# Kernel optimization log

Measured on AMD Instinct MI355X. Metric: run time of the kernel, lower is better.

The kernel has to match this reference:

```python
import jax, jax.numpy as jnp
import numpy as np

B, S, D, H = 4, 2048, 1024, 16
DH = D // H  # 64
R = 12       # random-projection rank forced by U's view()
EPS = 1e-6


def setup_inputs() -> dict:
    key = jax.random.key(0)
    ks = jax.random.split(key, 8)
    sc = 1.0 / np.sqrt(D)
    return {
        "Q": jax.random.normal(ks[0], (B, S, D), jnp.float32),
        "K": jax.random.normal(ks[1], (B, S, D), jnp.float32),
        "V": jax.random.normal(ks[2], (B, S, D), jnp.float32),
        "U": jax.random.normal(ks[3], (B, H, R, DH), jnp.float32),
        "W_Q": jax.random.normal(ks[4], (D, D), jnp.float32) * sc,
        "W_K": jax.random.normal(ks[5], (D, D), jnp.float32) * sc,
        "W_V": jax.random.normal(ks[6], (D, D), jnp.float32) * sc,
        "W_lin": jax.random.normal(ks[7], (D, D), jnp.float32) * sc,
        "b_lin": jnp.zeros((D,), jnp.float32),
        "gamma": jnp.ones((D,), jnp.float32),
        "beta": jnp.zeros((D,), jnp.float32),
    }


def reference(Q, K, V, U, W_Q, W_K, W_V, W_lin, b_lin, gamma, beta):
    b, s, d_model = Q.shape

    def proj(X, W):  # nn.Linear (no bias): X @ W^T, split heads -> [B,H,S,dh]
        return (X @ W.T).reshape(b, s, H, DH).transpose(0, 2, 1, 3)

    q = proj(Q, W_Q)
    k = proj(K, W_K)
    v = proj(V, W_V)

    # scores = (q @ U^T)^T @ k : random projection onto R=12 dims
    s1 = jnp.einsum('bhsd,bhrd->bhsr', q, U)          # [B,H,S,R]
    s2 = jnp.einsum('bhsr,bhsd->bhrd', s1, k)         # [B,H,R,dh]
    attn = jax.nn.softmax(s2, axis=-1)                # softmax over dh
    ctx = jnp.einsum('bhrd,bhsd->bhrs', attn, v)      # [B,H,R,S]
    # transpose(1,2) -> [B,R,H,S], flatten to [B, R*H*S/D, D]
    ctx = ctx.transpose(0, 2, 1, 3).reshape(b, -1, d_model)

    out = ctx @ W_lin.T + b_lin                       # final linear
    # dropout is identity in eval mode; then LayerNorm(eps=1e-6)
    mu = jnp.mean(out, axis=-1, keepdims=True)
    var = jnp.var(out, axis=-1, keepdims=True)
    return (out - mu) * jax.lax.rsqrt(var + EPS) * gamma + beta
```

## Files before the change

kernel.cpp:

```cpp
#include <hip/hip_runtime.h>

#define NB 4
#define NS 2048
#define ND 1024
#define NH 16
#define NDH 64
#define NR 12
#define NRH 192

typedef __attribute__((ext_vector_type(8))) short bf16x8;
typedef __attribute__((ext_vector_type(4))) float f32x4;

__device__ __forceinline__ unsigned short rnbf(float f) {
  unsigned u = __float_as_uint(f);
  u += 0x7fffu + ((u >> 16) & 1u);
  return (unsigned short)(u >> 16);
}
__device__ __forceinline__ float bf2f(unsigned short h) {
  return __uint_as_float(((unsigned)h) << 16);
}

__device__ __forceinline__ unsigned cvtpk(float a, float b) {
  unsigned r;
  asm("v_cvt_pk_bf16_f32 %0, %1, %2" : "=v"(r) : "v"(a), "v"(b));
  return r;
}
__device__ __forceinline__ uint4 pk_hi(float4 u, float4 w) {
  uint4 h;
  h.x = cvtpk(u.x, u.y); h.y = cvtpk(u.z, u.w);
  h.z = cvtpk(w.x, w.y); h.w = cvtpk(w.z, w.w);
  return h;
}
__device__ __forceinline__ unsigned lo2(float a, float b, unsigned hh) {
  float ah = __uint_as_float(hh << 16);
  float bh = __uint_as_float(hh & 0xffff0000u);
  return cvtpk(a - ah, b - bh);
}
__device__ __forceinline__ uint4 pk_lo(float4 u, float4 w, uint4 h) {
  uint4 l;
  l.x = lo2(u.x, u.y, h.x); l.y = lo2(u.z, u.w, h.y);
  l.z = lo2(w.x, w.y, h.z); l.w = lo2(w.z, w.w, h.w);
  return l;
}

__device__ __forceinline__ void gload16(const void* g, void* l) {
  __builtin_amdgcn_global_load_lds(
      (const __attribute__((address_space(1))) unsigned int*)g,
      (__attribute__((address_space(3))) unsigned int*)l, 16, 0, 0);
}

#define MFMA(a, b, c) __builtin_amdgcn_mfma_f32_16x16x32_bf16(a, b, c, 0, 0, 0)

__global__ __launch_bounds__(256) void transpose_k(const float* __restrict__ in,
                                                   float* __restrict__ out,
                                                   int rows, int cols) {
  __shared__ float tb[64][65];
  int r0 = blockIdx.y * 64, c0 = blockIdx.x * 64;
  int tx = threadIdx.x & 15, ty = threadIdx.x >> 4;
#pragma unroll
  for (int rr = 0; rr < 4; ++rr) {
    int row = ty + rr * 16;
    float4 v = *(const float4*)&in[(size_t)(r0 + row) * cols + c0 + tx * 4];
    tb[row][tx * 4 + 0] = v.x; tb[row][tx * 4 + 1] = v.y;
    tb[row][tx * 4 + 2] = v.z; tb[row][tx * 4 + 3] = v.w;
  }
  __syncthreads();
#pragma unroll
  for (int rr = 0; rr < 4; ++rr) {
    int orow = ty + rr * 16;
    float4 o;
    o.x = tb[tx * 4 + 0][orow];
    o.y = tb[tx * 4 + 1][orow];
    o.z = tb[tx * 4 + 2][orow];
    o.w = tb[tx * 4 + 3][orow];
    *(float4*)&out[(size_t)(c0 + orow) * rows + r0 + tx * 4] = o;
  }
}

__global__ __launch_bounds__(256) void build_wqeff(const float* __restrict__ U,
                                                   const float* __restrict__ WQ,
                                                   unsigned short* __restrict__ wqhi,
                                                   unsigned short* __restrict__ wqlo) {
  int idx = blockIdx.x;
  int hr = idx % (NH * NR);
  int h = hr / NR;
  __shared__ float u[NDH];
  int t = threadIdx.x;
  if (t < NDH) u[t] = U[(size_t)idx * NDH + t];
  __syncthreads();
  int e0 = t * 4;
  float a0 = 0.f, a1 = 0.f, a2 = 0.f, a3 = 0.f;
  const float* wbase = WQ + (size_t)h * NDH * ND + e0;
#pragma unroll 4
  for (int d = 0; d < NDH; ++d) {
    float uv = u[d];
    const float* wr = wbase + (size_t)d * ND;
    a0 += uv * wr[0]; a1 += uv * wr[1]; a2 += uv * wr[2]; a3 += uv * wr[3];
  }
  ushort4 h4, l4;
  h4.x = rnbf(a0); l4.x = rnbf(a0 - bf2f(h4.x));
  h4.y = rnbf(a1); l4.y = rnbf(a1 - bf2f(h4.y));
  h4.z = rnbf(a2); l4.z = rnbf(a2 - bf2f(h4.z));
  h4.w = rnbf(a3); l4.w = rnbf(a3 - bf2f(h4.w));
  *(ushort4*)&wqhi[(size_t)idx * ND + e0] = h4;
  *(ushort4*)&wqlo[(size_t)idx * ND + e0] = l4;
}

template <bool PAIR>
__global__ __launch_bounds__(256) void gemm_tn(
    const float* __restrict__ Af,
    const unsigned short* __restrict__ Bhi, const unsigned short* __restrict__ Blo,
    unsigned short* __restrict__ C0, unsigned short* __restrict__ C1) {
  constexpr int NBUF = PAIR ? 2 : 1;
  __shared__ unsigned short As[NBUF][64 * 64];
  __shared__ unsigned short Bs[NBUF][64 * 64];
  const int tid = threadIdx.x;
  const int lane = tid & 63;
  const int wid = tid >> 6;
  const int wm = wid >> 1, wn = wid & 1;
  const int m0 = blockIdx.x * 64, n0 = blockIdx.y * 64;
  const int b = blockIdx.z;
  const float* pA = Af + (size_t)b * NS * ND;
  const unsigned short* pBhi = Bhi + (size_t)b * NRH * ND;
  const unsigned short* pBlo = PAIR ? Blo + (size_t)b * NRH * ND : nullptr;

  const int rsub = lane >> 3;
  const int slot = (lane & 7) ^ rsub;
  const int arow = tid >> 2;
  const int jg = (tid & 3) * 2;

  f32x4 acc[2][2];
#pragma unroll
  for (int i = 0; i < 2; ++i)
#pragma unroll
    for (int j = 0; j < 2; ++j) acc[i][j] = (f32x4){0.f, 0.f, 0.f, 0.f};

  for (int k0 = 0; k0 < ND; k0 += 64) {
    const float* asrc = pA + (size_t)(m0 + arow) * ND + k0 + jg * 8;
    char* abase = (char*)&As[0][0] + arow * 128;
#pragma unroll
    for (int jj = 0; jj < 2; ++jj) {
      float4 u = *(const float4*)(asrc + jj * 8);
      float4 v = *(const float4*)(asrc + jj * 8 + 4);
      uint4 h = pk_hi(u, v);
      char* dst = abase + (((jg + jj) ^ (arow & 7)) << 4);
      *(uint4*)dst = h;
      if (PAIR) *(uint4*)(dst + 8192) = pk_lo(u, v, h);
    }
#pragma unroll
    for (int cc = 0; cc < 2; ++cc) {
      int c = wid * 2 + cc;
      int grow = n0 + c * 8 + rsub;
      gload16(&pBhi[(size_t)grow * ND + k0 + slot * 8], &Bs[0][c * 512]);
      if (PAIR)
        gload16(&pBlo[(size_t)grow * ND + k0 + slot * 8], &Bs[NBUF - 1][c * 512]);
    }
    __syncthreads();

#pragma unroll
    for (int kk = 0; kk < 64; kk += 32) {
      int sig = (kk >> 3) + (lane >> 4);
      bf16x8 ah[2], al[2], bh[2], bl[2];
#pragma unroll
      for (int fm = 0; fm < 2; ++fm) {
        int r = wm * 32 + fm * 16 + (lane & 15);
        int off = r * 128 + ((sig ^ (r & 7)) << 4);
        ah[fm] = *(const bf16x8*)((const char*)&As[0][0] + off);
        if (PAIR) al[fm] = *(const bf16x8*)((const char*)&As[0][0] + 8192 + off);
      }
#pragma unroll
      for (int fn = 0; fn < 2; ++fn) {
        int r = wn * 32 + fn * 16 + (lane & 15);
        int off = r * 128 + ((sig ^ (r & 7)) << 4);
        bh[fn] = *(const bf16x8*)((const char*)&Bs[0][0] + off);
        if (PAIR) bl[fn] = *(const bf16x8*)((const char*)&Bs[0][0] + 8192 + off);
      }
#pragma unroll
      for (int fm = 0; fm < 2; ++fm)
#pragma unroll
        for (int fn = 0; fn < 2; ++fn) {
          acc[fm][fn] = MFMA(ah[fm], bh[fn], acc[fm][fn]);
          if (PAIR) {
            acc[fm][fn] = MFMA(ah[fm], bl[fn], acc[fm][fn]);
            acc[fm][fn] = MFMA(al[fm], bh[fn], acc[fm][fn]);
          }
        }
    }
    __syncthreads();
  }

  const int jr = lane >> 4, cl = lane & 15;
#pragma unroll
  for (int fm = 0; fm < 2; ++fm)
#pragma unroll
    for (int fn = 0; fn < 2; ++fn) {
      f32x4 v = acc[fm][fn];
      int s = m0 + wm * 32 + fm * 16 + jr * 4;
      int rh = n0 + wn * 32 + fn * 16 + cl;
      int orow = PAIR ? rh : (rh % NR) * NH + rh / NR;
      size_t o = ((size_t)b * NRH + orow) * NS + s;
      ushort4 h4;
      h4.x = rnbf(v[0]); h4.y = rnbf(v[1]);
      h4.z = rnbf(v[2]); h4.w = rnbf(v[3]);
      *(ushort4*)&C0[o] = h4;
      if (PAIR) {
        ushort4 l4;
        l4.x = rnbf(v[0] - bf2f(h4.x)); l4.y = rnbf(v[1] - bf2f(h4.y));
        l4.z = rnbf(v[2] - bf2f(h4.z)); l4.w = rnbf(v[3] - bf2f(h4.w));
        *(ushort4*)&C1[o] = l4;
      }
    }
}

template <bool SPLIT, int BSRC, int BNT>
__global__ __launch_bounds__(256) void mgemm(
    const unsigned short* __restrict__ Ahi, const unsigned short* __restrict__ Alo,
    const float* __restrict__ Bf,
    float* __restrict__ P, int kchunk, int lda, int ldb, int ldc,
    long sAb, long sBb, long sPz, int nbatch) {
  constexpr int NBUF = SPLIT ? 2 : 1;
  constexpr int NFN = BNT / 32;
  __shared__ unsigned short As[NBUF][64 * 64];
  __shared__ unsigned short Bs[NBUF][BNT * 64];
  __shared__ float tbuf[(BSRC == 2) ? 64 * 68 : 4];
  const int tid = threadIdx.x;
  const int lane = tid & 63;
  const int wid = tid >> 6;
  const int wm = wid >> 1, wn = wid & 1;
  const int m0 = blockIdx.y * 64, n0 = blockIdx.x * BNT;
  const int bz = blockIdx.z;
  const int b = bz % nbatch;
  const int kbeg = (bz / nbatch) * kchunk;
  const unsigned short* pAhi = Ahi + (size_t)b * sAb;
  const unsigned short* pAlo = SPLIT ? (Alo + (size_t)b * sAb) : nullptr;
  const float* pBf = Bf + (size_t)b * sBb;

  const int rsub = lane >> 3;
  const int slot = (lane & 7) ^ rsub;

  f32x4 acc[2][NFN];
#pragma unroll
  for (int i = 0; i < 2; ++i)
#pragma unroll
    for (int j = 0; j < NFN; ++j) acc[i][j] = (f32x4){0.f, 0.f, 0.f, 0.f};

  for (int k0 = kbeg; k0 < kbeg + kchunk; k0 += 64) {
#pragma unroll
    for (int cc = 0; cc < 2; ++cc) {
      int c = wid * 2 + cc;
      int grow = m0 + c * 8 + rsub;
      gload16(&pAhi[(size_t)grow * lda + k0 + slot * 8], &As[0][c * 512]);
      if (SPLIT)
        gload16(&pAlo[(size_t)grow * lda + k0 + slot * 8], &As[NBUF - 1][c * 512]);
    }
    if constexpr (BSRC == 1) {
      const int brow = tid >> 1;
      const int jbase = (tid & 1) * 4;
      const float* bsrc = pBf + (size_t)(n0 + brow) * ldb + k0 + jbase * 8;
      char* dbase = (char*)&Bs[0][0] + brow * 128;
#pragma unroll
      for (int jj = 0; jj < 4; ++jj) {
        float4 u = *(const float4*)(bsrc + jj * 8);
        float4 w = *(const float4*)(bsrc + jj * 8 + 4);
        uint4 h = pk_hi(u, w);
        char* dst = dbase + (((jbase + jj) ^ (brow & 7)) << 4);
        *(uint4*)dst = h;
        if (SPLIT) *(uint4*)(dst + 2 * 64 * BNT) = pk_lo(u, w, h);
      }
      __syncthreads();
    } else {
      {
        const int sr = tid >> 2;
        const int eg = (tid & 3) * 16;
        const float* ksrc = pBf + (size_t)(k0 + sr) * ldb + n0 + eg;
        float* td = &tbuf[sr * 68 + eg];
        *(float4*)(td + 0)  = *(const float4*)(ksrc + 0);
        *(float4*)(td + 4)  = *(const float4*)(ksrc + 4);
        *(float4*)(td + 8)  = *(const float4*)(ksrc + 8);
        *(float4*)(td + 12) = *(const float4*)(ksrc + 12);
      }
      __syncthreads();
      {
        const int e = tid & 63;
        const int sg = (tid >> 6) * 16;
        float v[16];
#pragma unroll
        for (int i = 0; i < 16; ++i) v[i] = tbuf[(sg + i) * 68 + e];
        float4 u0 = {v[0], v[1], v[2], v[3]},   w0 = {v[4], v[5], v[6], v[7]};
        float4 u1 = {v[8], v[9], v[10], v[11]}, w1 = {v[12], v[13], v[14], v[15]};
        uint4 h0 = pk_hi(u0, w0), h1 = pk_hi(u1, w1);
        int j0 = sg >> 3;
        char* dbase = (char*)&Bs[0][0] + e * 128;
        *(uint4*)(dbase + (((j0 + 0) ^ (e & 7)) << 4)) = h0;
        *(uint4*)(dbase + (((j0 + 1) ^ (e & 7)) << 4)) = h1;
        if (SPLIT) {
          *(uint4*)(dbase + 2 * 64 * BNT + (((j0 + 0) ^ (e & 7)) << 4)) =
              pk_lo(u0, w0, h0);
          *(uint4*)(dbase + 2 * 64 * BNT + (((j0 + 1) ^ (e & 7)) << 4)) =
              pk_lo(u1, w1, h1);
        }
      }
      __syncthreads();
    }

#pragma unroll
    for (int kk = 0; kk < 64; kk += 32) {
      int sig = (kk >> 3) + (lane >> 4);
      bf16x8 ah[2], al[2], bh[NFN], bl[NFN];
#pragma unroll
      for (int fm = 0; fm < 2; ++fm) {
        int r = wm * 32 + fm * 16 + (lane & 15);
        int off = r * 128 + ((sig ^ (r & 7)) << 4);
        ah[fm] = *(const bf16x8*)((const char*)&As[0][0] + off);
        if (SPLIT) al[fm] = *(const bf16x8*)((const char*)&As[0][0] + 8192 + off);
      }
#pragma unroll
      for (int fn = 0; fn < NFN; ++fn) {
        int r = wn * (BNT / 2) + fn * 16 + (lane & 15);
        int off = r * 128 + ((sig ^ (r & 7)) << 4);
        bh[fn] = *(const bf16x8*)((const char*)&Bs[0][0] + off);
        if (SPLIT)
          bl[fn] = *(const bf16x8*)((const char*)&Bs[0][0] + 2 * 64 * BNT + off);
      }
#pragma unroll
      for (int fm = 0; fm < 2; ++fm)
#pragma unroll
        for (int fn = 0; fn < NFN; ++fn) {
          acc[fm][fn] = MFMA(ah[fm], bh[fn], acc[fm][fn]);
          if (SPLIT) {
            acc[fm][fn] = MFMA(ah[fm], bl[fn], acc[fm][fn]);
            acc[fm][fn] = MFMA(al[fm], bh[fn], acc[fm][fn]);
          }
        }
    }
    __syncthreads();
  }

  const int jr = lane >> 4, cl = lane & 15;
  float* pc = P + (size_t)bz * sPz;
#pragma unroll
  for (int fm = 0; fm < 2; ++fm)
#pragma unroll
    for (int fn = 0; fn < NFN; ++fn) {
      f32x4 v = acc[fm][fn];
      int gcol = n0 + wn * (BNT / 2) + fn * 16 + cl;
#pragma unroll
      for (int j = 0; j < 4; ++j) {
        int m = m0 + wm * 32 + fm * 16 + jr * 4 + j;
        pc[(size_t)m * ldc + gcol] = v[j];
      }
    }
}

__global__ __launch_bounds__(256) void red_bias_ln(const float* __restrict__ P,
                                                   const float* __restrict__ bias,
                                                   const float* __restrict__ gamma,
                                                   const float* __restrict__ beta,
                                                   float* __restrict__ out,
                                                   int nsplit) {
  int row = blockIdx.x;
  int t = threadIdx.x;
  const size_t slice = 1536 * (size_t)ND;
  float4 a = ((const float4*)(P + (size_t)row * ND))[t];
  for (int s = 1; s < nsplit; ++s) {
    float4 v = ((const float4*)(P + (size_t)s * slice + (size_t)row * ND))[t];
    a.x += v.x; a.y += v.y; a.z += v.z; a.w += v.w;
  }
  float4 bv = ((const float4*)bias)[t];
  a.x += bv.x; a.y += bv.y; a.z += bv.z; a.w += bv.w;

  float s = a.x + a.y + a.z + a.w;
  float ss = a.x * a.x + a.y * a.y + a.z * a.z + a.w * a.w;
#pragma unroll
  for (int off = 32; off > 0; off >>= 1) {
    s += __shfl_xor(s, off);
    ss += __shfl_xor(ss, off);
  }
  __shared__ float red[8];
  int wave = t >> 6, lane = t & 63;
  if (lane == 0) { red[wave] = s; red[4 + wave] = ss; }
  __syncthreads();
  s = red[0] + red[1] + red[2] + red[3];
  ss = red[4] + red[5] + red[6] + red[7];
  float mu = s * (1.0f / ND);
  float var = ss * (1.0f / ND) - mu * mu;
  float inv = rsqrtf(var + 1e-6f);
  float4 g = ((const float4*)gamma)[t];
  float4 be = ((const float4*)beta)[t];
  float4 o;
  o.x = (a.x - mu) * inv * g.x + be.x;
  o.y = (a.y - mu) * inv * g.y + be.y;
  o.z = (a.z - mu) * inv * g.z + be.z;
  o.w = (a.w - mu) * inv * g.w + be.w;
  ((float4*)(out + (size_t)row * ND))[t] = o;
}

__global__ __launch_bounds__(256) void sm_k(const float* __restrict__ P,
                                            int nsplit,
                                            const float* __restrict__ WKT,
                                            const float* __restrict__ WV,
                                            unsigned short* __restrict__ A2) {
  int x = blockIdx.x;
  int xcd = x & 7, within = x >> 3;
  int h = xcd + 8 * (within & 1);
  int rb = within >> 1;
  int r = rb >> 2, b = rb & 3;
  int idx = (b * NH + h) * NR + r;
  int rh = h * NR + r;

  const int t = threadIdx.x;
  __shared__ float t1s[ND];
  __shared__ float part[4][NDH];
  __shared__ float attns[NDH];

  {
    const size_t sstride = (size_t)NB * NRH * ND;
    const float* base = P + ((size_t)b * NRH + rh) * ND;
    float4 a = ((const float4*)base)[t];
    for (int s = 1; s < nsplit; ++s) {
      float4 v = ((const float4*)(base + (size_t)s * sstride))[t];
      a.x += v.x; a.y += v.y; a.z += v.z; a.w += v.w;
    }
    ((float4*)t1s)[t] = a;
  }
  __syncthreads();

  {
    int d = t & 63, q = t >> 6;
    const float* wcol = WKT + (size_t)(h * NDH + d);
    float acc = 0.f;
    int e0 = q * 256;
#pragma unroll 8
    for (int e = 0; e < 256; ++e)
      acc += t1s[e0 + e] * wcol[(size_t)(e0 + e) * ND];
    part[q][d] = acc;
  }
  __syncthreads();

  if (t < NDH) {
    float s2 = part[0][t] + part[1][t] + part[2][t] + part[3][t];
    float m = s2;
#pragma unroll
    for (int off = 32; off > 0; off >>= 1) m = fmaxf(m, __shfl_xor(m, off));
    float e = __expf(s2 - m);
    float sum = e;
#pragma unroll
    for (int off = 32; off > 0; off >>= 1) sum += __shfl_xor(sum, off);
    attns[t] = e / sum;
  }
  __syncthreads();

  {
    int e0 = t * 4;
    const float* wv = WV + (size_t)h * NDH * ND + e0;
    float a0 = 0.f, a1 = 0.f, a2 = 0.f, a3 = 0.f;
#pragma unroll 4
    for (int dd = 0; dd < NDH; ++dd) {
      float4 wvv = *(const float4*)&wv[(size_t)dd * ND];
      float a = attns[dd];
      a0 += a * wvv.x; a1 += a * wvv.y; a2 += a * wvv.z; a3 += a * wvv.w;
    }
    ushort4 o;
    o.x = rnbf(a0); o.y = rnbf(a1); o.z = rnbf(a2); o.w = rnbf(a3);
    *(ushort4*)&A2[(size_t)idx * ND + e0] = o;
  }
}

extern "C" void kernel_launch(void* const* d_in, const int* in_sizes, int n_in,
                              void* d_out, int out_size, void* d_ws, size_t ws_size,
                              hipStream_t stream) {
  const float* Q = (const float*)d_in[0];
  const float* K = (const float*)d_in[1];
  const float* V = (const float*)d_in[2];
  const float* U = (const float*)d_in[3];
  const float* WQ = (const float*)d_in[4];
  const float* WK = (const float*)d_in[5];
  const float* WV = (const float*)d_in[6];
  const float* WL = (const float*)d_in[7];
  const float* bl = (const float*)d_in[8];
  const float* ga = (const float*)d_in[9];
  const float* be = (const float*)d_in[10];
  float* out = (float*)d_out;
  char* w = (char*)d_ws;

  unsigned short* wqhi = (unsigned short*)w;
  unsigned short* wqlo = (unsigned short*)(w + 1572864);
  unsigned short* A2b = wqhi;
  unsigned short* s1hi = (unsigned short*)(w + 3145728);
  unsigned short* s1lo = (unsigned short*)(w + 6291456);
  unsigned short* ctxb = (unsigned short*)(w + 9437184);
  float* WKT = (float*)(w + 12582912);
  float* P = (float*)(w + 16777216);

  size_t avail = ws_size > 16777216 ? ws_size - 16777216 : 0;
  auto pick = [&](size_t bytesPerSplit, int maxs) {
    int s = 1;
    while (s * 2 <= maxs && bytesPerSplit * (size_t)(s * 2) <= avail) s *= 2;
    return s;
  };
  int sG2 = pick(3145728, 4);
  int sG4 = pick(6291456, 2);

  build_wqeff<<<NB * NH * NR, 256, 0, stream>>>(U, WQ, wqhi, wqlo);

  gemm_tn<true><<<dim3(32, 3, NB), 256, 0, stream>>>(
      Q, wqhi, wqlo, s1hi, s1lo);

  mgemm<true, 2, 64><<<dim3(16, 3, NB * sG2), 256, 0, stream>>>(
      s1hi, s1lo, K, P, 2048 / sG2,
      2048, 1024, 1024, 192L * 2048, 2048L * 1024, 192L * 1024, NB);

  transpose_k<<<dim3(16, 16), 256, 0, stream>>>(WK, WKT, ND, ND);

  sm_k<<<NB * NH * NR, 256, 0, stream>>>(P, sG2, WKT, WV, A2b);

  gemm_tn<false><<<dim3(32, 3, NB), 256, 0, stream>>>(
      V, A2b, nullptr, ctxb, nullptr);

  mgemm<false, 1, 128><<<dim3(8, 24, sG4), 256, 0, stream>>>(
      ctxb, nullptr, WL, P, 1024 / sG4,
      1024, 1024, 1024, 0, 0, 1536L * 1024, 1);
  red_bias_ln<<<1536, 256, 0, stream>>>(P, bl, ga, be, out, sG4);
}
```

Before: 130.4 us.

## Drop WK transpose, shrink GEMM tiles for occupancy, remove final split-K

Result: faster. 107.9 us (-17.3%).

```diff
diff --git a/kernel.cpp b/kernel.cpp
--- a/kernel.cpp
+++ b/kernel.cpp
@@ -50,32 +50,6 @@
 }
 
 #define MFMA(a, b, c) __builtin_amdgcn_mfma_f32_16x16x32_bf16(a, b, c, 0, 0, 0)
-
-__global__ __launch_bounds__(256) void transpose_k(const float* __restrict__ in,
-                                                   float* __restrict__ out,
-                                                   int rows, int cols) {
-  __shared__ float tb[64][65];
-  int r0 = blockIdx.y * 64, c0 = blockIdx.x * 64;
-  int tx = threadIdx.x & 15, ty = threadIdx.x >> 4;
-#pragma unroll
-  for (int rr = 0; rr < 4; ++rr) {
-    int row = ty + rr * 16;
-    float4 v = *(const float4*)&in[(size_t)(r0 + row) * cols + c0 + tx * 4];
-    tb[row][tx * 4 + 0] = v.x; tb[row][tx * 4 + 1] = v.y;
-    tb[row][tx * 4 + 2] = v.z; tb[row][tx * 4 + 3] = v.w;
-  }
-  __syncthreads();
-#pragma unroll
-  for (int rr = 0; rr < 4; ++rr) {
-    int orow = ty + rr * 16;
-    float4 o;
-    o.x = tb[tx * 4 + 0][orow];
-    o.y = tb[tx * 4 + 1][orow];
-    o.z = tb[tx * 4 + 2][orow];
-    o.w = tb[tx * 4 + 3][orow];
-    *(float4*)&out[(size_t)(c0 + orow) * rows + r0 + tx * 4] = o;
-  }
-}
 
 __global__ __launch_bounds__(256) void build_wqeff(const float* __restrict__ U,
                                                    const float* __restrict__ WQ,
@@ -106,19 +80,21 @@
   *(ushort4*)&wqlo[(size_t)idx * ND + e0] = l4;
 }
 
-template <bool PAIR>
+template <bool PAIR, int BMT>
 __global__ __launch_bounds__(256) void gemm_tn(
     const float* __restrict__ Af,
     const unsigned short* __restrict__ Bhi, const unsigned short* __restrict__ Blo,
     unsigned short* __restrict__ C0, unsigned short* __restrict__ C1) {
   constexpr int NBUF = PAIR ? 2 : 1;
-  __shared__ unsigned short As[NBUF][64 * 64];
+  constexpr int FM = BMT / 32;
+  constexpr int ALO = BMT * 128;
+  __shared__ unsigned short As[NBUF][BMT * 64];
   __shared__ unsigned short Bs[NBUF][64 * 64];
   const int tid = threadIdx.x;
   const int lane = tid & 63;
   const int wid = tid >> 6;
   const int wm = wid >> 1, wn = wid & 1;
-  const int m0 = blockIdx.x * 64, n0 = blockIdx.y * 64;
+  const int m0 = blockIdx.x * BMT, n0 = blockIdx.y * 64;
   const int b = blockIdx.z;
   const float* pA = Af + (size_t)b * NS * ND;
   const unsigned short* pBhi = Bhi + (size_t)b * NRH * ND;
@@ -126,26 +102,38 @@
 
   const int rsub = lane >> 3;
   const int slot = (lane & 7) ^ rsub;
-  const int arow = tid >> 2;
-  const int jg = (tid & 3) * 2;
-
-  f32x4 acc[2][2];
-#pragma unroll
-  for (int i = 0; i < 2; ++i)
+
+  f32x4 acc[FM][2];
+#pragma unroll
+  for (int i = 0; i < FM; ++i)
 #pragma unroll
     for (int j = 0; j < 2; ++j) acc[i][j] = (f32x4){0.f, 0.f, 0.f, 0.f};
 
   for (int k0 = 0; k0 < ND; k0 += 64) {
-    const float* asrc = pA + (size_t)(m0 + arow) * ND + k0 + jg * 8;
-    char* abase = (char*)&As[0][0] + arow * 128;
-#pragma unroll
-    for (int jj = 0; jj < 2; ++jj) {
-      float4 u = *(const float4*)(asrc + jj * 8);
-      float4 v = *(const float4*)(asrc + jj * 8 + 4);
+    if constexpr (BMT == 64) {
+      const int arow = tid >> 2;
+      const int jg = (tid & 3) * 2;
+      const float* asrc = pA + (size_t)(m0 + arow) * ND + k0 + jg * 8;
+      char* abase = (char*)&As[0][0] + arow * 128;
+#pragma unroll
+      for (int jj = 0; jj < 2; ++jj) {
+        float4 u = *(const float4*)(asrc + jj * 8);
+        float4 v = *(const float4*)(asrc + jj * 8 + 4);
+        uint4 h = pk_hi(u, v);
+        char* dst = abase + (((jg + jj) ^ (arow & 7)) << 4);
+        *(uint4*)dst = h;
+        if (PAIR) *(uint4*)(dst + ALO) = pk_lo(u, v, h);
+      }
+    } else {
+      const int arow = tid >> 3;
+      const int jg = tid & 7;
+      const float* asrc = pA + (size_t)(m0 + arow) * ND + k0 + jg * 8;
+      float4 u = *(const float4*)(asrc);
+      float4 v = *(const float4*)(asrc + 4);
       uint4 h = pk_hi(u, v);
-      char* dst = abase + (((jg + jj) ^ (arow & 7)) << 4);
+      char* dst = (char*)&As[0][0] + arow * 128 + ((jg ^ (arow & 7)) << 4);
       *(uint4*)dst = h;
-      if (PAIR) *(uint4*)(dst + 8192) = pk_lo(u, v, h);
+      if (PAIR) *(uint4*)(dst + ALO) = pk_lo(u, v, h);
     }
 #pragma unroll
     for (int cc = 0; cc < 2; ++cc) {
@@ -160,13 +148,13 @@
 #pragma unroll
     for (int kk = 0; kk < 64; kk += 32) {
       int sig = (kk >> 3) + (lane >> 4);
-      bf16x8 ah[2], al[2], bh[2], bl[2];
-#pragma unroll
-      for (int fm = 0; fm < 2; ++fm) {
-        int r = wm * 32 + fm * 16 + (lane & 15);
+      bf16x8 ah[FM], al[FM], bh[2], bl[2];
+#pragma unroll
+      for (int fm = 0; fm < FM; ++fm) {
+        int r = wm * (BMT / 2) + fm * 16 + (lane & 15);
         int off = r * 128 + ((sig ^ (r & 7)) << 4);
         ah[fm] = *(const bf16x8*)((const char*)&As[0][0] + off);
-        if (PAIR) al[fm] = *(const bf16x8*)((const char*)&As[0][0] + 8192 + off);
+        if (PAIR) al[fm] = *(const bf16x8*)((const char*)&As[0][0] + ALO + off);
       }
 #pragma unroll
       for (int fn = 0; fn < 2; ++fn) {
@@ -176,7 +164,7 @@
         if (PAIR) bl[fn] = *(const bf16x8*)((const char*)&Bs[0][0] + 8192 + off);
       }
 #pragma unroll
-      for (int fm = 0; fm < 2; ++fm)
+      for (int fm = 0; fm < FM; ++fm)
 #pragma unroll
         for (int fn = 0; fn < 2; ++fn) {
           acc[fm][fn] = MFMA(ah[fm], bh[fn], acc[fm][fn]);
@@ -191,11 +179,11 @@
 
   const int jr = lane >> 4, cl = lane & 15;
 #pragma unroll
-  for (int fm = 0; fm < 2; ++fm)
+  for (int fm = 0; fm < FM; ++fm)
 #pragma unroll
     for (int fn = 0; fn < 2; ++fn) {
       f32x4 v = acc[fm][fn];
-      int s = m0 + wm * 32 + fm * 16 + jr * 4;
+      int s = m0 + wm * (BMT / 2) + fm * 16 + jr * 4;
       int rh = n0 + wn * 32 + fn * 16 + cl;
       int orow = PAIR ? rh : (rh % NR) * NH + rh / NR;
       size_t o = ((size_t)b * NRH + orow) * NS + s;
@@ -254,18 +242,34 @@
         gload16(&pAlo[(size_t)grow * lda + k0 + slot * 8], &As[NBUF - 1][c * 512]);
     }
     if constexpr (BSRC == 1) {
-      const int brow = tid >> 1;
-      const int jbase = (tid & 1) * 4;
-      const float* bsrc = pBf + (size_t)(n0 + brow) * ldb + k0 + jbase * 8;
-      char* dbase = (char*)&Bs[0][0] + brow * 128;
-#pragma unroll
-      for (int jj = 0; jj < 4; ++jj) {
-        float4 u = *(const float4*)(bsrc + jj * 8);
-        float4 w = *(const float4*)(bsrc + jj * 8 + 4);
-        uint4 h = pk_hi(u, w);
-        char* dst = dbase + (((jbase + jj) ^ (brow & 7)) << 4);
-        *(uint4*)dst = h;
-        if (SPLIT) *(uint4*)(dst + 2 * 64 * BNT) = pk_lo(u, w, h);
+      if constexpr (BNT == 128) {
+        const int brow = tid >> 1;
+        const int jbase = (tid & 1) * 4;
+        const float* bsrc = pBf + (size_t)(n0 + brow) * ldb + k0 + jbase * 8;
+        char* dbase = (char*)&Bs[0][0] + brow * 128;
+#pragma unroll
+        for (int jj = 0; jj < 4; ++jj) {
+          float4 u = *(const float4*)(bsrc + jj * 8);
+          float4 w = *(const float4*)(bsrc + jj * 8 + 4);
+          uint4 h = pk_hi(u, w);
+          char* dst = dbase + (((jbase + jj) ^ (brow & 7)) << 4);
+          *(uint4*)dst = h;
+          if (SPLIT) *(uint4*)(dst + 2 * 64 * BNT) = pk_lo(u, w, h);
+        }
+      } else {
+        const int brow = tid >> 2;
+        const int jbase = (tid & 3) * 2;
+        const float* bsrc = pBf + (size_t)(n0 + brow) * ldb + k0 + jbase * 8;
+        char* dbase = (char*)&Bs[0][0] + brow * 128;
+#pragma unroll
+        for (int jj = 0; jj < 2; ++jj) {
+          float4 u = *(const float4*)(bsrc + jj * 8);
+          float4 w = *(const float4*)(bsrc + jj * 8 + 4);
+          uint4 h = pk_hi(u, w);
+          char* dst = dbase + (((jbase + jj) ^ (brow & 7)) << 4);
+          *(uint4*)dst = h;
+          if (SPLIT) *(uint4*)(dst + 2 * 64 * BNT) = pk_lo(u, w, h);
+        }
       }
       __syncthreads();
     } else {
@@ -352,20 +356,14 @@
     }
 }
 
-__global__ __launch_bounds__(256) void red_bias_ln(const float* __restrict__ P,
-                                                   const float* __restrict__ bias,
-                                                   const float* __restrict__ gamma,
-                                                   const float* __restrict__ beta,
-                                                   float* __restrict__ out,
-                                                   int nsplit) {
+__global__ __launch_bounds__(256) void bias_ln(const float* __restrict__ lin,
+                                               const float* __restrict__ bias,
+                                               const float* __restrict__ gamma,
+                                               const float* __restrict__ beta,
+                                               float* __restrict__ out) {
   int row = blockIdx.x;
   int t = threadIdx.x;
-  const size_t slice = 1536 * (size_t)ND;
-  float4 a = ((const float4*)(P + (size_t)row * ND))[t];
-  for (int s = 1; s < nsplit; ++s) {
-    float4 v = ((const float4*)(P + (size_t)s * slice + (size_t)row * ND))[t];
-    a.x += v.x; a.y += v.y; a.z += v.z; a.w += v.w;
-  }
+  float4 a = ((const float4*)(lin + (size_t)row * ND))[t];
   float4 bv = ((const float4*)bias)[t];
   a.x += bv.x; a.y += bv.y; a.z += bv.z; a.w += bv.w;
 
@@ -397,7 +395,7 @@
 
 __global__ __launch_bounds__(256) void sm_k(const float* __restrict__ P,
                                             int nsplit,
-                                            const float* __restrict__ WKT,
+                                            const float* __restrict__ WK,
                                             const float* __restrict__ WV,
                                             unsigned short* __restrict__ A2) {
   int x = blockIdx.x;
@@ -409,8 +407,9 @@
   int rh = h * NR + r;
 
   const int t = threadIdx.x;
+  const int lane = t & 63, wv = t >> 6;
   __shared__ float t1s[ND];
-  __shared__ float part[4][NDH];
+  __shared__ float s2s[NDH];
   __shared__ float attns[NDH];
 
   {
@@ -425,20 +424,20 @@
   }
   __syncthreads();
 
-  {
-    int d = t & 63, q = t >> 6;
-    const float* wcol = WKT + (size_t)(h * NDH + d);
+  for (int j = 0; j < 16; ++j) {
+    int d = wv * 16 + j;
+    const float* row = WK + (size_t)(h * NDH + d) * ND;
     float acc = 0.f;
-    int e0 = q * 256;
-#pragma unroll 8
-    for (int e = 0; e < 256; ++e)
-      acc += t1s[e0 + e] * wcol[(size_t)(e0 + e) * ND];
-    part[q][d] = acc;
+#pragma unroll
+    for (int i = 0; i < 16; ++i) acc += row[lane + i * 64] * t1s[lane + i * 64];
+#pragma unroll
+    for (int off = 32; off > 0; off >>= 1) acc += __shfl_xor(acc, off);
+    if (lane == 0) s2s[d] = acc;
   }
   __syncthreads();
 
   if (t < NDH) {
-    float s2 = part[0][t] + part[1][t] + part[2][t] + part[3][t];
+    float s2 = s2s[t];
     float m = s2;
 #pragma unroll
     for (int off = 32; off > 0; off >>= 1) m = fmaxf(m, __shfl_xor(m, off));
@@ -452,11 +451,11 @@
 
   {
     int e0 = t * 4;
-    const float* wv = WV + (size_t)h * NDH * ND + e0;
+    const float* wvp = WV + (size_t)h * NDH * ND + e0;
     float a0 = 0.f, a1 = 0.f, a2 = 0.f, a3 = 0.f;
 #pragma unroll 4
     for (int dd = 0; dd < NDH; ++dd) {
-      float4 wvv = *(const float4*)&wv[(size_t)dd * ND];
+      float4 wvv = *(const float4*)&wvp[(size_t)dd * ND];
       float a = attns[dd];
       a0 += a * wvv.x; a1 += a * wvv.y; a2 += a * wvv.z; a3 += a * wvv.w;
     }
@@ -489,36 +488,34 @@
   unsigned short* s1hi = (unsigned short*)(w + 3145728);
   unsigned short* s1lo = (unsigned short*)(w + 6291456);
   unsigned short* ctxb = (unsigned short*)(w + 9437184);
-  float* WKT = (float*)(w + 12582912);
-  float* P = (float*)(w + 16777216);
-
-  size_t avail = ws_size > 16777216 ? ws_size - 16777216 : 0;
+  float* lin = (float*)(w + 12582912);
+  float* P = (float*)(w + 18874368);
+
+  size_t avail = ws_size > 18874368 ? ws_size - 18874368 : 0;
   auto pick = [&](size_t bytesPerSplit, int maxs) {
     int s = 1;
     while (s * 2 <= maxs && bytesPerSplit * (size_t)(s * 2) <= avail) s *= 2;
     return s;
   };
   int sG2 = pick(3145728, 4);
-  int sG4 = pick(6291456, 2);
 
   build_wqeff<<<NB * NH * NR, 256, 0, stream>>>(U, WQ, wqhi, wqlo);
 
-  gemm_tn<true><<<dim3(32, 3, NB), 256, 0, stream>>>(
+  gemm_tn<true, 32><<<dim3(64, 3, NB), 256, 0, stream>>>(
       Q, wqhi, wqlo, s1hi, s1lo);
 
   mgemm<true, 2, 64><<<dim3(16, 3, NB * sG2), 256, 0, stream>>>(
       s1hi, s1lo, K, P, 2048 / sG2,
       2048, 1024, 1024, 192L * 2048, 2048L * 1024, 192L * 1024, NB);
 
-  transpose_k<<<dim3(16, 16), 256, 0, stream>>>(WK, WKT, ND, ND);
-
-  sm_k<<<NB * NH * NR, 256, 0, stream>>>(P, sG2, WKT, WV, A2b);
-
-  gemm_tn<false><<<dim3(32, 3, NB), 256, 0, stream>>>(
+  sm_k<<<NB * NH * NR, 256, 0, stream>>>(P, sG2, WK, WV, A2b);
+
+  gemm_tn<false, 32><<<dim3(64, 3, NB), 256, 0, stream>>>(
       V, A2b, nullptr, ctxb, nullptr);
 
-  mgemm<false, 1, 128><<<dim3(8, 24, sG4), 256, 0, stream>>>(
-      ctxb, nullptr, WL, P, 1024 / sG4,
-      1024, 1024, 1024, 0, 0, 1536L * 1024, 1);
-  red_bias_ln<<<1536, 256, 0, stream>>>(P, bl, ga, be, out, sG4);
-}
+  mgemm<false, 1, 64><<<dim3(16, 24, 1), 256, 0, stream>>>(
+      ctxb, nullptr, WL, lin, 1024,
+      1024, 1024, 1024, 0, 0, 0, 1);
+
+  bias_ln<<<1536, 256, 0, stream>>>(lin, bl, ga, be, out);
+}
```
